# Kernel tuning notes

Measured on AMD Instinct MI355X. Metric: run time of the kernel, lower is better.

The kernel has to match this reference:

```python
import jax, jax.numpy as jnp
import numpy as np

D_MODEL, D_K, D_V = 512, 64, 64
LN_EPS = 1e-6


def setup_inputs() -> dict:
    key = jax.random.key(0)
    ks = jax.random.split(key, 8)
    B, Lq, Lk = 2, 1024, 1024
    q = jax.random.normal(ks[0], (B, Lq, D_MODEL), dtype=jnp.float32)
    k = jax.random.normal(ks[1], (B, Lk, D_MODEL), dtype=jnp.float32)
    v = jax.random.normal(ks[2], (B, Lk, D_MODEL), dtype=jnp.float32)
    s = 1.0 / np.sqrt(D_MODEL)
    Wq = jax.random.normal(ks[3], (D_MODEL, D_K), dtype=jnp.float32) * s
    Wk = jax.random.normal(ks[4], (D_MODEL, D_K), dtype=jnp.float32) * s
    Wv = jax.random.normal(ks[5], (D_MODEL, D_V), dtype=jnp.float32) * s
    v_param = jax.random.normal(ks[6], (D_K,), dtype=jnp.float32)
    Wfc = jax.random.normal(ks[7], (D_V, D_MODEL), dtype=jnp.float32) / np.sqrt(D_V)
    ln_gamma = jnp.ones((D_MODEL,), dtype=jnp.float32)
    ln_beta = jnp.zeros((D_MODEL,), dtype=jnp.float32)
    return {"q": q, "k": k, "v": v, "Wq": Wq, "Wk": Wk, "Wv": Wv,
            "v_param": v_param, "Wfc": Wfc, "ln_gamma": ln_gamma, "ln_beta": ln_beta}


def reference(q, k, v, Wq, Wk, Wv, v_param, Wfc, ln_gamma, ln_beta):
    residual = q
    qp = q @ Wq                      # [B, Lq, d_k]
    kp = k @ Wk                      # [B, Lk, d_k]
    vp = v @ Wv                      # [B, Lk, d_v]
    # additive (Bahdanau) scores: tanh(q_i + k_j) . v_param  -> [B, Lq, Lk]
    scores = jnp.einsum("bqkd,d->bqk", jnp.tanh(qp[:, :, None, :] + kp[:, None, :, :]), v_param)
    attn = jax.nn.softmax(scores, axis=-1)   # dropout is identity in eval mode
    out = jnp.einsum("bqk,bkv->bqv", attn, vp)
    out = out @ Wfc + residual               # [B, Lq, d_model]
    mu = jnp.mean(out, axis=-1, keepdims=True)
    var = jnp.var(out, axis=-1, keepdims=True)
    out = (out - mu) * jax.lax.rsqrt(var + LN_EPS) * ln_gamma + ln_beta
    return out, attn
```

## Files before the change

### kernel.cpp

```cpp
#include <hip/hip_runtime.h>
#include <cstddef>
#include <cstdint>

#define D_MODEL 512
#define DK 64
#define LQ 1024
#define LK 1024
#define NB 2
#define LN_EPS 1e-6f
#define L2E2 2.8853900817779268f

__device__ __forceinline__ uint32_t pack_bf2(float a, float b) {
  uint32_t ua = __float_as_uint(a), ub = __float_as_uint(b);
  ua = (ua + 0x7fffu + ((ua >> 16) & 1u)) >> 16;
  ub = (ub + 0x7fffu + ((ub >> 16) & 1u)) >> 16;
  return (ub << 16) | ua;
}

#define PR_ROWS 8
__global__ __launch_bounds__(256, 4) void proj_kernel(
    const float* __restrict__ q, const float* __restrict__ k,
    const float* __restrict__ v, const float* __restrict__ Wq,
    const float* __restrict__ Wk, const float* __restrict__ Wv,
    const float* __restrict__ v_param, float2* __restrict__ ab_g,
    uint32_t* __restrict__ ekT, float* __restrict__ vp) {
  __shared__ float rows[PR_ROWS][D_MODEL];
  const int tid = threadIdx.x;
  const int type = blockIdx.x >> 8;
  const int r0 = (blockIdx.x & 255) * PR_ROWS;
  const float* __restrict__ in = (type == 0) ? q : (type == 1) ? k : v;
  const float* __restrict__ W = (type == 0) ? Wq : (type == 1) ? Wk : Wv;
  {
    const float4* __restrict__ in4 = (const float4*)(in + (size_t)r0 * D_MODEL);
    float4* r4 = (float4*)&rows[0][0];
#pragma unroll
    for (int t = 0; t < 4; ++t) r4[tid + 256 * t] = in4[tid + 256 * t];
  }
  __syncthreads();
  const int lane = tid & 63;
  const int wv = tid >> 6;
  const int rglob = r0 + wv * 2;
  const float* __restrict__ Wl = W + lane;
  const float* __restrict__ rA = rows[wv * 2];
  const float* __restrict__ rB = rows[wv * 2 + 1];
  float c0a = 0.f, c1a = 0.f, c0b = 0.f, c1b = 0.f;
#pragma unroll 2
  for (int e = 0; e < D_MODEL; e += 4) {
    float w0 = Wl[(size_t)(e + 0) * DK];
    float w1 = Wl[(size_t)(e + 1) * DK];
    float w2 = Wl[(size_t)(e + 2) * DK];
    float w3 = Wl[(size_t)(e + 3) * DK];
    float4 xa = *(const float4*)&rA[e];
    float4 xb = *(const float4*)&rB[e];
    c0a = fmaf(xa.x, w0, c0a); c1a = fmaf(xa.y, w1, c1a);
    c0a = fmaf(xa.z, w2, c0a); c1a = fmaf(xa.w, w3, c1a);
    c0b = fmaf(xb.x, w0, c0b); c1b = fmaf(xb.y, w1, c1b);
    c0b = fmaf(xb.z, w2, c0b); c1b = fmaf(xb.w, w3, c1b);
  }
  float acc0 = c0a + c1a, acc1 = c0b + c1b;
  if (type == 0) {
    float vpar = v_param[lane];
    float i0 = __builtin_amdgcn_exp2f(-L2E2 * acc0);
    float i1 = __builtin_amdgcn_exp2f(-L2E2 * acc1);
    ab_g[(size_t)(rglob + 0) * DK + lane] = make_float2(vpar * i0, i0);
    ab_g[(size_t)(rglob + 1) * DK + lane] = make_float2(vpar * i1, i1);
  } else if (type == 1) {
    float e0 = __builtin_amdgcn_exp2f(L2E2 * acc0);
    float e1 = __builtin_amdgcn_exp2f(L2E2 * acc1);
    float h0 = __shfl_down(e0, 32);
    float h1 = __shfl_down(e1, 32);
    if (lane < 32) {
      int b = rglob >> 10, j0 = rglob & 1023;
      uint2 pk;
      pk.x = pack_bf2(e0, h0);
      pk.y = pack_bf2(e1, h1);
      *(uint2*)&ekT[(size_t)b * 32 * LK + (size_t)lane * LK + j0] = pk;
    }
  } else {
    vp[(size_t)(rglob + 0) * DK + lane] = acc0;
    vp[(size_t)(rglob + 1) * DK + lane] = acc1;
  }
}

#define RB 8
__global__ __launch_bounds__(512, 4) void attn_kernel(
    const float2* __restrict__ ab_g, const uint32_t* __restrict__ ekT,
    const float* __restrict__ vp, const float* __restrict__ resid,
    const float* __restrict__ Wfc, const float* __restrict__ gamma,
    const float* __restrict__ beta, float* __restrict__ out,
    float* __restrict__ attn_out) {
  __shared__ float sc[RB][LK];
  __shared__ float4 ab4s[RB][32];
  __shared__ float4 pvred[8][RB][16];
  __shared__ __align__(16) float ovlT[DK][RB];
  __shared__ float red[2][RB][8];
  const int tid = threadIdx.x;
  const int row0 = blockIdx.x * RB;
  const int batch = row0 >> 10;
  const uint32_t* __restrict__ ekT_b = ekT + (size_t)batch * 32 * LK;
  const float* __restrict__ vp_b = vp + (size_t)batch * LK * DK;

  {
    int r = tid >> 6, d = tid & 63;
    float2 abv = ab_g[(size_t)(row0 + r) * DK + d];
    ((float2*)&ab4s[r][d & 31])[d >> 5] = abv;
  }
  __syncthreads();

  {
    float acc0[RB], acc1[RB];
#pragma unroll
    for (int r = 0; r < RB; ++r) { acc0[r] = 0.f; acc1[r] = 0.f; }
#pragma unroll 4
    for (int dp = 0; dp < 32; ++dp) {
      uint32_t kw0 = ekT_b[(size_t)dp * LK + tid];
      uint32_t kw1 = ekT_b[(size_t)dp * LK + tid + 512];
      float klo0 = __uint_as_float(kw0 << 16);
      float khi0 = __uint_as_float(kw0 & 0xffff0000u);
      float klo1 = __uint_as_float(kw1 << 16);
      float khi1 = __uint_as_float(kw1 & 0xffff0000u);
#pragma unroll
      for (int r = 0; r < RB; ++r) {
        float4 ab = ab4s[r][dp];
        float x1 = klo0 + ab.y, x2 = khi0 + ab.w;
        float n0 = fmaf(ab.z, x1, ab.x * x2);
        acc0[r] = fmaf(n0, __builtin_amdgcn_rcpf(x1 * x2), acc0[r]);
        float y1 = klo1 + ab.y, y2 = khi1 + ab.w;
        float n1 = fmaf(ab.z, y1, ab.x * y2);
        acc1[r] = fmaf(n1, __builtin_amdgcn_rcpf(y1 * y2), acc1[r]);
      }
    }
#pragma unroll
    for (int r = 0; r < RB; ++r) {
      sc[r][tid] = acc0[r];
      sc[r][tid + 512] = acc1[r];
    }
  }
  __syncthreads();

  const int wave = __builtin_amdgcn_readfirstlane(tid >> 6);
  const int lane = tid & 63;

  {
    const int r = wave;
    float m = 1e30f;
#pragma unroll
    for (int i = 0; i < 16; ++i) m = fminf(m, sc[r][i * 64 + lane]);
#pragma unroll
    for (int off = 32; off > 0; off >>= 1) m = fminf(m, __shfl_xor(m, off));
    float p[16];
    float ssum = 0.f;
#pragma unroll
    for (int i = 0; i < 16; ++i) {
      float e = __builtin_amdgcn_exp2f((m - sc[r][i * 64 + lane]) * L2E2);
      p[i] = e;
      ssum += e;
    }
#pragma unroll
    for (int off = 32; off > 0; off >>= 1) ssum += __shfl_xor(ssum, off);
    float inv = __builtin_amdgcn_rcpf(ssum);
    float* __restrict__ arow = attn_out + (size_t)(row0 + r) * LK;
#pragma unroll
    for (int i = 0; i < 16; ++i) {
      float pn = p[i] * inv;
      sc[r][i * 64 + lane] = pn;
      arow[i * 64 + lane] = pn;
    }
  }
  __syncthreads();

  {
    const int jj = lane >> 4, l16 = lane & 15;
    const float4* __restrict__ vp4 = (const float4*)vp_b;
    float4 a[RB];
#pragma unroll
    for (int r = 0; r < RB; ++r) a[r] = make_float4(0.f, 0.f, 0.f, 0.f);
#pragma unroll 2
    for (int it = 0; it < 32; ++it) {
      int j = (wave << 7) + (it << 2) + jj;
      float4 vv = vp4[(size_t)j * (DK / 4) + l16];
#pragma unroll
      for (int r = 0; r < RB; ++r) {
        float pw = sc[r][j];
        a[r].x = fmaf(pw, vv.x, a[r].x);
        a[r].y = fmaf(pw, vv.y, a[r].y);
        a[r].z = fmaf(pw, vv.z, a[r].z);
        a[r].w = fmaf(pw, vv.w, a[r].w);
      }
    }
#pragma unroll
    for (int r = 0; r < RB; ++r) {
      a[r].x += __shfl_xor(a[r].x, 16); a[r].y += __shfl_xor(a[r].y, 16);
      a[r].z += __shfl_xor(a[r].z, 16); a[r].w += __shfl_xor(a[r].w, 16);
      a[r].x += __shfl_xor(a[r].x, 32); a[r].y += __shfl_xor(a[r].y, 32);
      a[r].z += __shfl_xor(a[r].z, 32); a[r].w += __shfl_xor(a[r].w, 32);
    }
    if (jj == 0) {
#pragma unroll
      for (int r = 0; r < RB; ++r) pvred[wave][r][l16] = a[r];
    }
  }
  __syncthreads();
  if (tid < 128) {
    int r = tid >> 4, l16 = tid & 15;
    float4 s = make_float4(0.f, 0.f, 0.f, 0.f);
#pragma unroll
    for (int w = 0; w < 8; ++w) {
      float4 t = pvred[w][r][l16];
      s.x += t.x; s.y += t.y; s.z += t.z; s.w += t.w;
    }
    ovlT[l16 * 4 + 0][r] = s.x;
    ovlT[l16 * 4 + 1][r] = s.y;
    ovlT[l16 * 4 + 2][r] = s.z;
    ovlT[l16 * 4 + 3][r] = s.w;
  }
  __syncthreads();

  {
    const int c = tid;
    float y[RB];
#pragma unroll
    for (int r = 0; r < RB; ++r)
      y[r] = resid[(size_t)(row0 + r) * D_MODEL + c];
#pragma unroll 4
    for (int e = 0; e < DK; ++e) {
      float w = Wfc[(size_t)e * D_MODEL + c];
      float4 o0 = *(const float4*)&ovlT[e][0];
      float4 o1 = *(const float4*)&ovlT[e][4];
      y[0] = fmaf(o0.x, w, y[0]); y[1] = fmaf(o0.y, w, y[1]);
      y[2] = fmaf(o0.z, w, y[2]); y[3] = fmaf(o0.w, w, y[3]);
      y[4] = fmaf(o1.x, w, y[4]); y[5] = fmaf(o1.y, w, y[5]);
      y[6] = fmaf(o1.z, w, y[6]); y[7] = fmaf(o1.w, w, y[7]);
    }
#pragma unroll
    for (int r = 0; r < RB; ++r) {
      float s = y[r];
#pragma unroll
      for (int off = 32; off > 0; off >>= 1) s += __shfl_xor(s, off);
      if (lane == 0) red[0][r][wave] = s;
    }
    __syncthreads();
    float mu[RB];
#pragma unroll
    for (int r = 0; r < RB; ++r) {
      float s = 0.f;
#pragma unroll
      for (int w = 0; w < 8; ++w) s += red[0][r][w];
      mu[r] = s * (1.0f / D_MODEL);
    }
#pragma unroll
    for (int r = 0; r < RB; ++r) {
      float d = y[r] - mu[r];
      float s = d * d;
#pragma unroll
      for (int off = 32; off > 0; off >>= 1) s += __shfl_xor(s, off);
      if (lane == 0) red[1][r][wave] = s;
    }
    __syncthreads();
    float gg = gamma[c], bb = beta[c];
#pragma unroll
    for (int r = 0; r < RB; ++r) {
      float s = 0.f;
#pragma unroll
      for (int w = 0; w < 8; ++w) s += red[1][r][w];
      float var = s * (1.0f / D_MODEL);
      float rstd = rsqrtf(var + LN_EPS);
      out[(size_t)(row0 + r) * D_MODEL + c] = (y[r] - mu[r]) * rstd * gg + bb;
    }
  }
}

extern "C" void kernel_launch(void* const* d_in, const int* in_sizes, int n_in,
                              void* d_out, int out_size, void* d_ws,
                              size_t ws_size, hipStream_t stream) {
  const float* q = (const float*)d_in[0];
  const float* k = (const float*)d_in[1];
  const float* v = (const float*)d_in[2];
  const float* Wq = (const float*)d_in[3];
  const float* Wk = (const float*)d_in[4];
  const float* Wv = (const float*)d_in[5];
  const float* v_param = (const float*)d_in[6];
  const float* Wfc = (const float*)d_in[7];
  const float* gamma = (const float*)d_in[8];
  const float* beta = (const float*)d_in[9];

  float* out = (float*)d_out;
  float* attn = out + (size_t)NB * LQ * D_MODEL;

  float* base = (float*)d_ws;
  float2* ab_g = (float2*)base;
  uint32_t* ekT = (uint32_t*)(base + (size_t)2 * NB * LQ * DK);
  float* vp = base + (size_t)2 * NB * LQ * DK + NB * 32 * LK;

  hipLaunchKernelGGL(proj_kernel, dim3(3 * 256), dim3(256), 0, stream, q, k, v,
                     Wq, Wk, Wv, v_param, ab_g, ekT, vp);
  hipLaunchKernelGGL(attn_kernel, dim3(NB * LQ / RB), dim3(512), 0, stream,
                     ab_g, ekT, vp, q, Wfc, gamma, beta, out, attn);
}
```

Measured before the change: 60.11 us.

## Split fused attention kernel into score/softmax and PV+FC+LayerNorm kernels

Breaks the single attention kernel into a score kernel that computes scores and softmax in registers with 2 rows per 256-thread block, and a second kernel that rereads the attn output from global memory for PV, the output projection and LayerNorm with 4 rows per block. The aim is more blocks and better occupancy in each phase, and dropping the large shared score buffer from the score phase. In exchange it adds a kernel launch and a global-memory round trip of the 8MB attn matrix, and each block now reuses the ekT and vp reads across fewer rows.

```diff
diff --git a/kernel.cpp b/kernel.cpp
--- a/kernel.cpp
+++ b/kernel.cpp
@@ -82,105 +82,127 @@
   }
 }
 
-#define RB 8
-__global__ __launch_bounds__(512, 4) void attn_kernel(
+#define RB 2
+__global__ __launch_bounds__(256, 4) void score_kernel(
     const float2* __restrict__ ab_g, const uint32_t* __restrict__ ekT,
-    const float* __restrict__ vp, const float* __restrict__ resid,
-    const float* __restrict__ Wfc, const float* __restrict__ gamma,
-    const float* __restrict__ beta, float* __restrict__ out,
     float* __restrict__ attn_out) {
-  __shared__ float sc[RB][LK];
   __shared__ float4 ab4s[RB][32];
-  __shared__ float4 pvred[8][RB][16];
-  __shared__ __align__(16) float ovlT[DK][RB];
-  __shared__ float red[2][RB][8];
+  __shared__ float mred[RB][4], sred[RB][4];
   const int tid = threadIdx.x;
   const int row0 = blockIdx.x * RB;
   const int batch = row0 >> 10;
   const uint32_t* __restrict__ ekT_b = ekT + (size_t)batch * 32 * LK;
-  const float* __restrict__ vp_b = vp + (size_t)batch * LK * DK;
-
-  {
+  if (tid < RB * 64) {
     int r = tid >> 6, d = tid & 63;
     float2 abv = ab_g[(size_t)(row0 + r) * DK + d];
     ((float2*)&ab4s[r][d & 31])[d >> 5] = abv;
   }
   __syncthreads();
 
-  {
-    float acc0[RB], acc1[RB];
-#pragma unroll
-    for (int r = 0; r < RB; ++r) { acc0[r] = 0.f; acc1[r] = 0.f; }
-#pragma unroll 4
-    for (int dp = 0; dp < 32; ++dp) {
-      uint32_t kw0 = ekT_b[(size_t)dp * LK + tid];
-      uint32_t kw1 = ekT_b[(size_t)dp * LK + tid + 512];
-      float klo0 = __uint_as_float(kw0 << 16);
-      float khi0 = __uint_as_float(kw0 & 0xffff0000u);
-      float klo1 = __uint_as_float(kw1 << 16);
-      float khi1 = __uint_as_float(kw1 & 0xffff0000u);
-#pragma unroll
-      for (int r = 0; r < RB; ++r) {
-        float4 ab = ab4s[r][dp];
-        float x1 = klo0 + ab.y, x2 = khi0 + ab.w;
-        float n0 = fmaf(ab.z, x1, ab.x * x2);
-        acc0[r] = fmaf(n0, __builtin_amdgcn_rcpf(x1 * x2), acc0[r]);
-        float y1 = klo1 + ab.y, y2 = khi1 + ab.w;
-        float n1 = fmaf(ab.z, y1, ab.x * y2);
-        acc1[r] = fmaf(n1, __builtin_amdgcn_rcpf(y1 * y2), acc1[r]);
+  float acc[RB][4];
+#pragma unroll
+  for (int r = 0; r < RB; ++r)
+#pragma unroll
+    for (int jj = 0; jj < 4; ++jj) acc[r][jj] = 0.f;
+
+#pragma unroll 2
+  for (int dp = 0; dp < 32; ++dp) {
+    float klo[4], khi[4];
+#pragma unroll
+    for (int jj = 0; jj < 4; ++jj) {
+      uint32_t kw = ekT_b[(size_t)dp * LK + tid + jj * 256];
+      klo[jj] = __uint_as_float(kw << 16);
+      khi[jj] = __uint_as_float(kw & 0xffff0000u);
+    }
+#pragma unroll
+    for (int r = 0; r < RB; ++r) {
+      float4 ab = ab4s[r][dp];
+#pragma unroll
+      for (int jj = 0; jj < 4; ++jj) {
+        float x1 = klo[jj] + ab.y, x2 = khi[jj] + ab.w;
+        float num = fmaf(ab.z, x1, ab.x * x2);
+        acc[r][jj] = fmaf(num, __builtin_amdgcn_rcpf(x1 * x2), acc[r][jj]);
       }
     }
-#pragma unroll
-    for (int r = 0; r < RB; ++r) {
-      sc[r][tid] = acc0[r];
-      sc[r][tid + 512] = acc1[r];
-    }
-  }
-  __syncthreads();
+  }
 
   const int wave = __builtin_amdgcn_readfirstlane(tid >> 6);
   const int lane = tid & 63;
 
   {
-    const int r = wave;
-    float m = 1e30f;
-#pragma unroll
-    for (int i = 0; i < 16; ++i) m = fminf(m, sc[r][i * 64 + lane]);
-#pragma unroll
-    for (int off = 32; off > 0; off >>= 1) m = fminf(m, __shfl_xor(m, off));
-    float p[16];
-    float ssum = 0.f;
-#pragma unroll
-    for (int i = 0; i < 16; ++i) {
-      float e = __builtin_amdgcn_exp2f((m - sc[r][i * 64 + lane]) * L2E2);
-      p[i] = e;
-      ssum += e;
-    }
-#pragma unroll
-    for (int off = 32; off > 0; off >>= 1) ssum += __shfl_xor(ssum, off);
-    float inv = __builtin_amdgcn_rcpf(ssum);
-    float* __restrict__ arow = attn_out + (size_t)(row0 + r) * LK;
-#pragma unroll
-    for (int i = 0; i < 16; ++i) {
-      float pn = p[i] * inv;
-      sc[r][i * 64 + lane] = pn;
-      arow[i * 64 + lane] = pn;
-    }
-  }
-  __syncthreads();
+#pragma unroll
+    for (int r = 0; r < RB; ++r) {
+      float pm = fminf(fminf(acc[r][0], acc[r][1]), fminf(acc[r][2], acc[r][3]));
+#pragma unroll
+      for (int off = 32; off > 0; off >>= 1) pm = fminf(pm, __shfl_xor(pm, off));
+      if (lane == 0) mred[r][wave] = pm;
+    }
+    __syncthreads();
+#pragma unroll
+    for (int r = 0; r < RB; ++r) {
+      float m = fminf(fminf(mred[r][0], mred[r][1]),
+                      fminf(mred[r][2], mred[r][3]));
+      float s = 0.f;
+#pragma unroll
+      for (int jj = 0; jj < 4; ++jj) {
+        float e = __builtin_amdgcn_exp2f((m - acc[r][jj]) * L2E2);
+        acc[r][jj] = e;
+        s += e;
+      }
+#pragma unroll
+      for (int off = 32; off > 0; off >>= 1) s += __shfl_xor(s, off);
+      if (lane == 0) sred[r][wave] = s;
+    }
+    __syncthreads();
+#pragma unroll
+    for (int r = 0; r < RB; ++r) {
+      float inv = __builtin_amdgcn_rcpf(sred[r][0] + sred[r][1] + sred[r][2] +
+                                        sred[r][3]);
+      float* __restrict__ arow = attn_out + (size_t)(row0 + r) * LK;
+#pragma unroll
+      for (int jj = 0; jj < 4; ++jj)
+        arow[tid + jj * 256] = acc[r][jj] * inv;
+    }
+  }
+}
+
+#define PRB 4
+__global__ __launch_bounds__(512, 4) void pvfc_kernel(
+    const float* __restrict__ attn, const float* __restrict__ vp,
+    const float* __restrict__ resid, const float* __restrict__ Wfc,
+    const float* __restrict__ gamma, const float* __restrict__ beta,
+    float* __restrict__ out) {
+  __shared__ float sc[PRB][LK];
+  __shared__ float4 pvred[8][PRB][16];
+  __shared__ __align__(16) float ovlT[DK][PRB];
+  __shared__ float red[2][PRB][8];
+  const int tid = threadIdx.x;
+  const int row0 = blockIdx.x * PRB;
+  const int batch = row0 >> 10;
+  const float* __restrict__ vp_b = vp + (size_t)batch * LK * DK;
+  {
+    const float4* __restrict__ a4 = (const float4*)(attn + (size_t)row0 * LK);
+    float4* s4 = (float4*)&sc[0][0];
+#pragma unroll
+    for (int t = 0; t < 2; ++t) s4[tid + 512 * t] = a4[tid + 512 * t];
+  }
+  __syncthreads();
+
+  const int wave = __builtin_amdgcn_readfirstlane(tid >> 6);
+  const int lane = tid & 63;
 
   {
     const int jj = lane >> 4, l16 = lane & 15;
     const float4* __restrict__ vp4 = (const float4*)vp_b;
-    float4 a[RB];
-#pragma unroll
-    for (int r = 0; r < RB; ++r) a[r] = make_float4(0.f, 0.f, 0.f, 0.f);
-#pragma unroll 2
+    float4 a[PRB];
+#pragma unroll
+    for (int r = 0; r < PRB; ++r) a[r] = make_float4(0.f, 0.f, 0.f, 0.f);
+#pragma unroll 4
     for (int it = 0; it < 32; ++it) {
       int j = (wave << 7) + (it << 2) + jj;
       float4 vv = vp4[(size_t)j * (DK / 4) + l16];
 #pragma unroll
-      for (int r = 0; r < RB; ++r) {
+      for (int r = 0; r < PRB; ++r) {
         float pw = sc[r][j];
         a[r].x = fmaf(pw, vv.x, a[r].x);
         a[r].y = fmaf(pw, vv.y, a[r].y);
@@ -189,7 +211,7 @@
       }
     }
 #pragma unroll
-    for (int r = 0; r < RB; ++r) {
+    for (int r = 0; r < PRB; ++r) {
       a[r].x += __shfl_xor(a[r].x, 16); a[r].y += __shfl_xor(a[r].y, 16);
       a[r].z += __shfl_xor(a[r].z, 16); a[r].w += __shfl_xor(a[r].w, 16);
       a[r].x += __shfl_xor(a[r].x, 32); a[r].y += __shfl_xor(a[r].y, 32);
@@ -197,11 +219,11 @@
     }
     if (jj == 0) {
 #pragma unroll
-      for (int r = 0; r < RB; ++r) pvred[wave][r][l16] = a[r];
-    }
-  }
-  __syncthreads();
-  if (tid < 128) {
+      for (int r = 0; r < PRB; ++r) pvred[wave][r][l16] = a[r];
+    }
+  }
+  __syncthreads();
+  if (tid < 64) {
     int r = tid >> 4, l16 = tid & 15;
     float4 s = make_float4(0.f, 0.f, 0.f, 0.f);
 #pragma unroll
@@ -218,38 +240,37 @@
 
   {
     const int c = tid;
-    float y[RB];
-#pragma unroll
-    for (int r = 0; r < RB; ++r)
+    float y[PRB];
+#pragma unroll
+    for (int r = 0; r < PRB; ++r)
       y[r] = resid[(size_t)(row0 + r) * D_MODEL + c];
 #pragma unroll 4
     for (int e = 0; e < DK; ++e) {
       float w = Wfc[(size_t)e * D_MODEL + c];
-      float4 o0 = *(const float4*)&ovlT[e][0];
-      float4 o1 = *(const float4*)&ovlT[e][4];
-      y[0] = fmaf(o0.x, w, y[0]); y[1] = fmaf(o0.y, w, y[1]);
-      y[2] = fmaf(o0.z, w, y[2]); y[3] = fmaf(o0.w, w, y[3]);
-      y[4] = fmaf(o1.x, w, y[4]); y[5] = fmaf(o1.y, w, y[5]);
-      y[6] = fmaf(o1.z, w, y[6]); y[7] = fmaf(o1.w, w, y[7]);
-    }
-#pragma unroll
-    for (int r = 0; r < RB; ++r) {
+      float4 ov = *(const float4*)&ovlT[e][0];
+      y[0] = fmaf(ov.x, w, y[0]);
+      y[1] = fmaf(ov.y, w, y[1]);
+      y[2] = fmaf(ov.z, w, y[2]);
+      y[3] = fmaf(ov.w, w, y[3]);
+    }
+#pragma unroll
+    for (int r = 0; r < PRB; ++r) {
       float s = y[r];
 #pragma unroll
       for (int off = 32; off > 0; off >>= 1) s += __shfl_xor(s, off);
       if (lane == 0) red[0][r][wave] = s;
     }
     __syncthreads();
-    float mu[RB];
-#pragma unroll
-    for (int r = 0; r < RB; ++r) {
+    float mu[PRB];
+#pragma unroll
+    for (int r = 0; r < PRB; ++r) {
       float s = 0.f;
 #pragma unroll
       for (int w = 0; w < 8; ++w) s += red[0][r][w];
       mu[r] = s * (1.0f / D_MODEL);
     }
 #pragma unroll
-    for (int r = 0; r < RB; ++r) {
+    for (int r = 0; r < PRB; ++r) {
       float d = y[r] - mu[r];
       float s = d * d;
 #pragma unroll
@@ -259,7 +280,7 @@
     __syncthreads();
     float gg = gamma[c], bb = beta[c];
 #pragma unroll
-    for (int r = 0; r < RB; ++r) {
+    for (int r = 0; r < PRB; ++r) {
       float s = 0.f;
 #pragma unroll
       for (int w = 0; w < 8; ++w) s += red[1][r][w];
@@ -294,6 +315,8 @@
 
   hipLaunchKernelGGL(proj_kernel, dim3(3 * 256), dim3(256), 0, stream, q, k, v,
                      Wq, Wk, Wv, v_param, ab_g, ekT, vp);
-  hipLaunchKernelGGL(attn_kernel, dim3(NB * LQ / RB), dim3(512), 0, stream,
-                     ab_g, ekT, vp, q, Wfc, gamma, beta, out, attn);
-}
+  hipLaunchKernelGGL(score_kernel, dim3(NB * LQ / RB), dim3(256), 0, stream,
+                     ab_g, ekT, attn);
+  hipLaunchKernelGGL(pvfc_kernel, dim3(NB * LQ / PRB), dim3(512), 0, stream,
+                     attn, vp, q, Wfc, gamma, beta, out);
+}
```

After: 65.29 us. +8.6%, slower.
